# Optimization experiments

Hardware: AMD Instinct MI355X
Metric: run time of the kernel (lower is better)

Reference implementation:

```python
import jax, jax.numpy as jnp
import numpy as np

TARGET_KAPPA = 1.0 / 61.0
EPS = 1e-10

# --- antisymmetric expansion: 35 independent components (i<j<k) -> (7,7,7) ---
_combos = np.array([(i, j, k) for i in range(7) for j in range(i + 1, 7) for k in range(j + 1, 7)])  # (35,3)
_perm_specs = [((0, 1, 2), 1.0), ((0, 2, 1), -1.0), ((1, 0, 2), -1.0), ((1, 2, 0), 1.0), ((2, 0, 1), 1.0), ((2, 1, 0), -1.0)]
_I = jnp.array(np.concatenate([_combos[:, p[0]] for p, _ in _perm_specs]))
_J = jnp.array(np.concatenate([_combos[:, p[1]] for p, _ in _perm_specs]))
_K = jnp.array(np.concatenate([_combos[:, p[2]] for p, _ in _perm_specs]))
_S = jnp.array(np.concatenate([np.full(35, s, dtype=np.float32) for _, s in _perm_specs]))


def expand_to_antisymmetric(v35):
    # v35: (35,) -> antisymmetric (7,7,7)
    vals = jnp.tile(v35, 6) * _S.astype(v35.dtype)
    return jnp.zeros((7, 7, 7), v35.dtype).at[_I, _J, _K].set(vals)


def _phi_single(xi, W1, b1, W2, b2):
    # xi: (7,) -> antisymmetric 3-form (7,7,7)
    h = jnp.tanh(xi @ W1 + b1)          # (H,)
    v35 = h @ W2 + b2                    # (35,)
    return expand_to_antisymmetric(v35)


def setup_inputs() -> dict:
    key = jax.random.key(0)
    k1, k2, k3 = jax.random.split(key, 3)
    B, H = 32768, 512
    x = jax.random.normal(k1, (B, 7), dtype=jnp.float32)
    W1 = jax.random.normal(k2, (7, H), dtype=jnp.float32) * 0.3
    b1 = jnp.zeros((H,), dtype=jnp.float32)
    W2 = jax.random.normal(k3, (H, 35), dtype=jnp.float32) * 0.05
    b2 = jnp.zeros((35,), dtype=jnp.float32)
    return {"x": x, "W1": W1, "b1": b1, "W2": W2, "b2": b2}


def reference(x, W1, b1, W2, b2):
    f = lambda xi: _phi_single(xi, W1, b1, W2, b2)
    # Jacobian replaces the 35 looped autograd.grad calls: (B,7,7,7,7), last axis = d/dx_l
    jac = jax.vmap(jax.jacfwd(f))(x)
    d_phi = jnp.moveaxis(jac, -1, 1)  # (B, 7(deriv), 7, 7, 7), matching torch layout
    torsion_sq = jnp.sum(d_phi ** 2, axis=(1, 2, 3, 4))  # (B,)
    torsion_norm = jnp.sqrt(torsion_sq + EPS)
    loss = jnp.mean((torsion_norm - TARGET_KAPPA) ** 2)
    return loss, jnp.mean(torsion_norm)
```

## Files before the change

### kernel.cpp

```cpp
#include <hip/hip_runtime.h>
#include <hip/hip_bf16.h>
#include <math.h>

typedef __attribute__((ext_vector_type(8)))  short bf16x8;
typedef __attribute__((ext_vector_type(16))) float f32x16;
typedef unsigned int u32;

#define KAPPA (1.0f/61.0f)
#define NBLK 512

__device__ __forceinline__ unsigned short f2bf(float f) {
    u32 x = __float_as_uint(f);
    x += 0x7fffu + ((x >> 16) & 1u);
    return (unsigned short)(x >> 16);
}
__device__ __forceinline__ float fast_rcp(float v) {
#if __has_builtin(__builtin_amdgcn_rcpf)
    return __builtin_amdgcn_rcpf(v);
#else
    return 1.0f / v;
#endif
}
__device__ __forceinline__ u32 pack_bf16(float lo, float hi) {
    __hip_bfloat162 p = __float22bfloat162_rn(make_float2(lo, hi));
    return *reinterpret_cast<u32*>(&p);
}

__global__ void build_v(const float* __restrict__ W1, const float* __restrict__ W2,
                        const float* __restrict__ b1,
                        bf16x8* __restrict__ V, bf16x8* __restrict__ Wt) {
    int t = blockIdx.x * blockDim.x + threadIdx.x;
    if (t < 16384) {
        int lane = t & 63, ptile = (t >> 6) & 7, kkg = t >> 9;
        int p  = ptile * 32 + (lane & 31);
        int hb = kkg * 16 + (lane >> 5) * 8;
        bool valid = (p < 245);
        int l7 = valid ? p / 35 : 0;
        int c  = valid ? p - l7 * 35 : 0;
        bf16x8 v;
#pragma unroll
        for (int i = 0; i < 8; ++i) {
            int h = hb + i;
            v[i] = valid ? (short)f2bf(W1[l7 * 512 + h] * W2[h * 35 + c]) : (short)0;
        }
        V[t] = v;
    } else if (t < 16384 + 1024) {
        int f = t - 16384;
        int lane = f & 63, htile = f >> 6;
        int h = htile * 32 + (lane & 31);
        bf16x8 v;
#pragma unroll
        for (int i = 0; i < 8; ++i) v[i] = 0;
        if (lane < 32) {
#pragma unroll
            for (int l = 0; l < 7; ++l) v[l] = (short)f2bf(W1[l * 512 + h]);
            v[7] = (short)f2bf(b1[h]);
        }
        Wt[f] = v;
    }
}

__global__ __launch_bounds__(256, 3)
void torsion_main(const float* __restrict__ x,
                  const bf16x8* __restrict__ V, const bf16x8* __restrict__ Wt,
                  float* __restrict__ partials) {
    __shared__ __align__(16) u32 Gb[2][8][64 * 4];
    __shared__ float red[4][2][32];

    const int tid  = threadIdx.x;
    const int lane = tid & 63;
    const int w    = tid >> 6;
    const int blk  = blockIdx.x;
    const int rt   = w & 1;
    const int ht   = w >> 1;

    bf16x8 xf;
#pragma unroll
    for (int i = 0; i < 8; ++i) xf[i] = 0;
    if (lane < 32) {
        const float* xp = x + ((size_t)blk * 64 + rt * 32 + lane) * 7;
#pragma unroll
        for (int l = 0; l < 7; ++l) xf[l] = (short)f2bf(xp[l]);
        xf[7] = (short)f2bf(1.0f);
    }

    f32x16 acc[2][2];
#pragma unroll
    for (int pt = 0; pt < 2; ++pt)
#pragma unroll
        for (int r2 = 0; r2 < 2; ++r2)
#pragma unroll
            for (int e = 0; e < 16; ++e) acc[pt][r2][e] = 0.0f;

    auto pre_pack = [&](int c, u32 d[8]) {
        bf16x8 wf = Wt[(c * 2 + ht) * 64 + lane];
        f32x16 p;
#pragma unroll
        for (int e = 0; e < 16; ++e) p[e] = 0.0f;
        p = __builtin_amdgcn_mfma_f32_32x32x16_bf16(wf, xf, p, 0, 0, 0);
#pragma unroll
        for (int j = 0; j < 8; ++j) {
            float t0 = __expf(-2.0f * fabsf(p[2 * j]));
            float r0 = fast_rcp(1.0f + t0);
            float g0 = 4.0f * t0 * r0 * r0;
            float t1 = __expf(-2.0f * fabsf(p[2 * j + 1]));
            float r1 = fast_rcp(1.0f + t1);
            float g1 = 4.0f * t1 * r1 * r1;
            d[j] = pack_bf16(g0, g1);
        }
    };
    auto store_g = [&](int buf, const u32 d[8]) {
        const int f0  = 4 * ht + rt;
        const int f1  = f0 + 2;
        const int col = lane & 31;
        const int hw2 = (lane >> 5) << 1;
        *reinterpret_cast<uint2*>(&Gb[buf][f0][(col     ) * 4 + hw2]) = make_uint2(d[0], d[1]);
        *reinterpret_cast<uint2*>(&Gb[buf][f0][(col + 32) * 4 + hw2]) = make_uint2(d[2], d[3]);
        *reinterpret_cast<uint2*>(&Gb[buf][f1][(col     ) * 4 + hw2]) = make_uint2(d[4], d[5]);
        *reinterpret_cast<uint2*>(&Gb[buf][f1][(col + 32) * 4 + hw2]) = make_uint2(d[6], d[7]);
    };

    {
        u32 d0[8];
        pre_pack(0, d0);
        store_g(0, d0);
    }
    __syncthreads();

    for (int c = 0; c < 8; ++c) {
        const int buf = c & 1;

        bf16x8 vreg[8];
#pragma unroll
        for (int ks = 0; ks < 4; ++ks) {
            const int fb = ((c * 4 + ks) * 8 + 2 * w) * 64 + lane;
            vreg[2 * ks]     = V[fb];
            vreg[2 * ks + 1] = V[fb + 64];
        }

        u32 dn[8];
        if (c < 7) pre_pack(c + 1, dn);

        __builtin_amdgcn_s_setprio(1);
#pragma unroll
        for (int ks = 0; ks < 4; ++ks) {
            bf16x8 g0 = *reinterpret_cast<const bf16x8*>(&Gb[buf][ks * 2 + 0][lane * 4]);
            bf16x8 g1 = *reinterpret_cast<const bf16x8*>(&Gb[buf][ks * 2 + 1][lane * 4]);
            acc[0][0] = __builtin_amdgcn_mfma_f32_32x32x16_bf16(vreg[2 * ks],     g0, acc[0][0], 0, 0, 0);
            acc[0][1] = __builtin_amdgcn_mfma_f32_32x32x16_bf16(vreg[2 * ks],     g1, acc[0][1], 0, 0, 0);
            acc[1][0] = __builtin_amdgcn_mfma_f32_32x32x16_bf16(vreg[2 * ks + 1], g0, acc[1][0], 0, 0, 0);
            acc[1][1] = __builtin_amdgcn_mfma_f32_32x32x16_bf16(vreg[2 * ks + 1], g1, acc[1][1], 0, 0, 0);
        }
        __builtin_amdgcn_s_setprio(0);

        if (c < 7) store_g(buf ^ 1, dn);
        __syncthreads();
    }

#pragma unroll
    for (int r2 = 0; r2 < 2; ++r2) {
        float s = 0.0f;
#pragma unroll
        for (int pt = 0; pt < 2; ++pt)
#pragma unroll
            for (int e = 0; e < 16; ++e) s += acc[pt][r2][e] * acc[pt][r2][e];
        s += __shfl_xor(s, 32);
        if (lane < 32) red[w][r2][lane] = s;
    }
    __syncthreads();

    if (tid < 64) {
        const int li = tid & 31, rr = tid >> 5;
        float q = 6.0f * (red[0][rr][li] + red[1][rr][li] + red[2][rr][li] + red[3][rr][li]);
        float n = sqrtf(q + 1e-10f);
        float d = n - KAPPA;
        float a = d * d, b = n;
#pragma unroll
        for (int m = 1; m <= 32; m <<= 1) {
            a += __shfl_xor(a, m);
            b += __shfl_xor(b, m);
        }
        if (tid == 0) {
            partials[blk]        = a;
            partials[NBLK + blk] = b;
        }
    }
}

__global__ void finalize_k(const float* __restrict__ partials, float* __restrict__ out) {
    __shared__ float sl[256], sn[256];
    int tid = threadIdx.x;
    sl[tid] = partials[tid] + partials[tid + 256];
    sn[tid] = partials[NBLK + tid] + partials[NBLK + tid + 256];
    __syncthreads();
    for (int st = 128; st > 0; st >>= 1) {
        if (tid < st) { sl[tid] += sl[tid + st]; sn[tid] += sn[tid + st]; }
        __syncthreads();
    }
    if (tid == 0) {
        out[0] = sl[0] / 32768.0f;
        out[1] = sn[0] / 32768.0f;
    }
}

extern "C" void kernel_launch(void* const* d_in, const int* in_sizes, int n_in,
                              void* d_out, int out_size, void* d_ws, size_t ws_size,
                              hipStream_t stream) {
    const float* x  = (const float*)d_in[0];
    const float* W1 = (const float*)d_in[1];
    const float* b1 = (const float*)d_in[2];
    const float* W2 = (const float*)d_in[3];

    bf16x8* V        = (bf16x8*)d_ws;
    bf16x8* Wt       = V + 16384;
    float*  partials = (float*)(Wt + 1024);

    build_v<<<68, 256, 0, stream>>>(W1, W2, b1, V, Wt);
    torsion_main<<<NBLK, 256, 0, stream>>>(x, V, Wt, partials);
    finalize_k<<<1, 256, 0, stream>>>(partials, (float*)d_out);
}
```

Baseline: 25.71 us.

## Double rows per block, reuse V fragments across four row tiles, prefetch V/Wt

Measured after the change: 25.92 us. Within noise of the previous version (+0.8%).

```diff
diff --git a/kernel.cpp b/kernel.cpp
--- a/kernel.cpp
+++ b/kernel.cpp
@@ -7,7 +7,8 @@
 typedef unsigned int u32;
 
 #define KAPPA (1.0f/61.0f)
-#define NBLK 512
+#define NBLK 256
+#define SWAP23(r) (((r) & 19) | (((r) & 4) << 1) | (((r) & 8) >> 1))
 
 __device__ __forceinline__ unsigned short f2bf(float f) {
     u32 x = __float_as_uint(f);
@@ -47,7 +48,8 @@
     } else if (t < 16384 + 1024) {
         int f = t - 16384;
         int lane = f & 63, htile = f >> 6;
-        int h = htile * 32 + (lane & 31);
+        int row = lane & 31;
+        int h = htile * 32 + SWAP23(row);
         bf16x8 v;
 #pragma unroll
         for (int i = 0; i < 8; ++i) v[i] = 0;
@@ -60,44 +62,38 @@
     }
 }
 
-__global__ __launch_bounds__(256, 3)
+__global__ __launch_bounds__(256, 1)
 void torsion_main(const float* __restrict__ x,
                   const bf16x8* __restrict__ V, const bf16x8* __restrict__ Wt,
                   float* __restrict__ partials) {
-    __shared__ __align__(16) u32 Gb[2][8][64 * 4];
-    __shared__ float red[4][2][32];
+    __shared__ __align__(16) u32 Gb[2][16][64 * 4];
+    __shared__ float red[4][4][32];
+    __shared__ float fin[2][2];
 
     const int tid  = threadIdx.x;
     const int lane = tid & 63;
     const int w    = tid >> 6;
     const int blk  = blockIdx.x;
-    const int rt   = w & 1;
-    const int ht   = w >> 1;
 
     bf16x8 xf;
 #pragma unroll
     for (int i = 0; i < 8; ++i) xf[i] = 0;
     if (lane < 32) {
-        const float* xp = x + ((size_t)blk * 64 + rt * 32 + lane) * 7;
+        const float* xp = x + ((size_t)blk * 128 + w * 32 + lane) * 7;
 #pragma unroll
         for (int l = 0; l < 7; ++l) xf[l] = (short)f2bf(xp[l]);
         xf[7] = (short)f2bf(1.0f);
     }
 
-    f32x16 acc[2][2];
+    f32x16 acc[2][4];
 #pragma unroll
     for (int pt = 0; pt < 2; ++pt)
 #pragma unroll
-        for (int r2 = 0; r2 < 2; ++r2)
-#pragma unroll
-            for (int e = 0; e < 16; ++e) acc[pt][r2][e] = 0.0f;
-
-    auto pre_pack = [&](int c, u32 d[8]) {
-        bf16x8 wf = Wt[(c * 2 + ht) * 64 + lane];
-        f32x16 p;
-#pragma unroll
-        for (int e = 0; e < 16; ++e) p[e] = 0.0f;
-        p = __builtin_amdgcn_mfma_f32_32x32x16_bf16(wf, xf, p, 0, 0, 0);
+        for (int st = 0; st < 4; ++st)
+#pragma unroll
+            for (int e = 0; e < 16; ++e) acc[pt][st][e] = 0.0f;
+
+    auto compute_g = [&](const f32x16& p, u32 d[8]) {
 #pragma unroll
         for (int j = 0; j < 8; ++j) {
             float t0 = __expf(-2.0f * fabsf(p[2 * j]));
@@ -109,89 +105,119 @@
             d[j] = pack_bf16(g0, g1);
         }
     };
-    auto store_g = [&](int buf, const u32 d[8]) {
-        const int f0  = 4 * ht + rt;
-        const int f1  = f0 + 2;
-        const int col = lane & 31;
-        const int hw2 = (lane >> 5) << 1;
-        *reinterpret_cast<uint2*>(&Gb[buf][f0][(col     ) * 4 + hw2]) = make_uint2(d[0], d[1]);
-        *reinterpret_cast<uint2*>(&Gb[buf][f0][(col + 32) * 4 + hw2]) = make_uint2(d[2], d[3]);
-        *reinterpret_cast<uint2*>(&Gb[buf][f1][(col     ) * 4 + hw2]) = make_uint2(d[4], d[5]);
-        *reinterpret_cast<uint2*>(&Gb[buf][f1][(col + 32) * 4 + hw2]) = make_uint2(d[6], d[7]);
-    };
-
+
+    bf16x8 wt0 = Wt[0 * 64 + lane];
+    bf16x8 wt1 = Wt[1 * 64 + lane];
     {
-        u32 d0[8];
-        pre_pack(0, d0);
-        store_g(0, d0);
-    }
+        f32x16 p0, p1;
+#pragma unroll
+        for (int e = 0; e < 16; ++e) { p0[e] = 0.0f; p1[e] = 0.0f; }
+        p0 = __builtin_amdgcn_mfma_f32_32x32x16_bf16(wt0, xf, p0, 0, 0, 0);
+        p1 = __builtin_amdgcn_mfma_f32_32x32x16_bf16(wt1, xf, p1, 0, 0, 0);
+        u32 d0[8], d1[8];
+        compute_g(p0, d0);
+        compute_g(p1, d1);
+        *reinterpret_cast<uint4*>(&Gb[0][0 * 4 + w][lane * 4]) = make_uint4(d0[0], d0[1], d0[2], d0[3]);
+        *reinterpret_cast<uint4*>(&Gb[0][1 * 4 + w][lane * 4]) = make_uint4(d0[4], d0[5], d0[6], d0[7]);
+        *reinterpret_cast<uint4*>(&Gb[0][2 * 4 + w][lane * 4]) = make_uint4(d1[0], d1[1], d1[2], d1[3]);
+        *reinterpret_cast<uint4*>(&Gb[0][3 * 4 + w][lane * 4]) = make_uint4(d1[4], d1[5], d1[6], d1[7]);
+    }
+    bf16x8 vr[8];
+#pragma unroll
+    for (int ks = 0; ks < 4; ++ks) {
+        const int fb = (ks * 8 + 2 * w) * 64 + lane;
+        vr[ks * 2]     = V[fb];
+        vr[ks * 2 + 1] = V[fb + 64];
+    }
+    wt0 = Wt[2 * 64 + lane];
+    wt1 = Wt[3 * 64 + lane];
     __syncthreads();
 
     for (int c = 0; c < 8; ++c) {
         const int buf = c & 1;
 
-        bf16x8 vreg[8];
-#pragma unroll
-        for (int ks = 0; ks < 4; ++ks) {
-            const int fb = ((c * 4 + ks) * 8 + 2 * w) * 64 + lane;
-            vreg[2 * ks]     = V[fb];
-            vreg[2 * ks + 1] = V[fb + 64];
-        }
-
-        u32 dn[8];
-        if (c < 7) pre_pack(c + 1, dn);
-
-        __builtin_amdgcn_s_setprio(1);
-#pragma unroll
-        for (int ks = 0; ks < 4; ++ks) {
-            bf16x8 g0 = *reinterpret_cast<const bf16x8*>(&Gb[buf][ks * 2 + 0][lane * 4]);
-            bf16x8 g1 = *reinterpret_cast<const bf16x8*>(&Gb[buf][ks * 2 + 1][lane * 4]);
-            acc[0][0] = __builtin_amdgcn_mfma_f32_32x32x16_bf16(vreg[2 * ks],     g0, acc[0][0], 0, 0, 0);
-            acc[0][1] = __builtin_amdgcn_mfma_f32_32x32x16_bf16(vreg[2 * ks],     g1, acc[0][1], 0, 0, 0);
-            acc[1][0] = __builtin_amdgcn_mfma_f32_32x32x16_bf16(vreg[2 * ks + 1], g0, acc[1][0], 0, 0, 0);
-            acc[1][1] = __builtin_amdgcn_mfma_f32_32x32x16_bf16(vreg[2 * ks + 1], g1, acc[1][1], 0, 0, 0);
-        }
-        __builtin_amdgcn_s_setprio(0);
-
-        if (c < 7) store_g(buf ^ 1, dn);
+        f32x16 p0, p1;
+        if (c < 7) {
+#pragma unroll
+            for (int e = 0; e < 16; ++e) { p0[e] = 0.0f; p1[e] = 0.0f; }
+            p0 = __builtin_amdgcn_mfma_f32_32x32x16_bf16(wt0, xf, p0, 0, 0, 0);
+            p1 = __builtin_amdgcn_mfma_f32_32x32x16_bf16(wt1, xf, p1, 0, 0, 0);
+        }
+
+#pragma unroll
+        for (int ks = 0; ks < 4; ++ks)
+#pragma unroll
+            for (int st = 0; st < 4; ++st) {
+                bf16x8 g = *reinterpret_cast<const bf16x8*>(&Gb[buf][ks * 4 + st][lane * 4]);
+                acc[0][st] = __builtin_amdgcn_mfma_f32_32x32x16_bf16(vr[ks * 2],     g, acc[0][st], 0, 0, 0);
+                acc[1][st] = __builtin_amdgcn_mfma_f32_32x32x16_bf16(vr[ks * 2 + 1], g, acc[1][st], 0, 0, 0);
+            }
+
+        if (c < 7) {
+#pragma unroll
+            for (int ks = 0; ks < 4; ++ks) {
+                const int fb = (((c + 1) * 4 + ks) * 8 + 2 * w) * 64 + lane;
+                vr[ks * 2]     = V[fb];
+                vr[ks * 2 + 1] = V[fb + 64];
+            }
+        }
+        if (c < 6) {
+            wt0 = Wt[((c + 2) * 2 + 0) * 64 + lane];
+            wt1 = Wt[((c + 2) * 2 + 1) * 64 + lane];
+        }
+
+        if (c < 7) {
+            u32 d0[8], d1[8];
+            compute_g(p0, d0);
+            compute_g(p1, d1);
+            *reinterpret_cast<uint4*>(&Gb[buf ^ 1][0 * 4 + w][lane * 4]) = make_uint4(d0[0], d0[1], d0[2], d0[3]);
+            *reinterpret_cast<uint4*>(&Gb[buf ^ 1][1 * 4 + w][lane * 4]) = make_uint4(d0[4], d0[5], d0[6], d0[7]);
+            *reinterpret_cast<uint4*>(&Gb[buf ^ 1][2 * 4 + w][lane * 4]) = make_uint4(d1[0], d1[1], d1[2], d1[3]);
+            *reinterpret_cast<uint4*>(&Gb[buf ^ 1][3 * 4 + w][lane * 4]) = make_uint4(d1[4], d1[5], d1[6], d1[7]);
+        }
         __syncthreads();
     }
 
 #pragma unroll
-    for (int r2 = 0; r2 < 2; ++r2) {
+    for (int st = 0; st < 4; ++st) {
         float s = 0.0f;
 #pragma unroll
         for (int pt = 0; pt < 2; ++pt)
 #pragma unroll
-            for (int e = 0; e < 16; ++e) s += acc[pt][r2][e] * acc[pt][r2][e];
+            for (int e = 0; e < 16; ++e) s += acc[pt][st][e] * acc[pt][st][e];
         s += __shfl_xor(s, 32);
-        if (lane < 32) red[w][r2][lane] = s;
-    }
-    __syncthreads();
-
-    if (tid < 64) {
-        const int li = tid & 31, rr = tid >> 5;
-        float q = 6.0f * (red[0][rr][li] + red[1][rr][li] + red[2][rr][li] + red[3][rr][li]);
+        if (lane < 32) red[w][st][lane] = s;
+    }
+    __syncthreads();
+
+    if (tid < 128) {
+        const int st = tid >> 5, col = tid & 31;
+        float q = 6.0f * (red[0][st][col] + red[1][st][col] + red[2][st][col] + red[3][st][col]);
         float n = sqrtf(q + 1e-10f);
-        float d = n - KAPPA;
-        float a = d * d, b = n;
+        float dd = n - KAPPA;
+        float a = dd * dd, b = n;
 #pragma unroll
         for (int m = 1; m <= 32; m <<= 1) {
             a += __shfl_xor(a, m);
             b += __shfl_xor(b, m);
         }
-        if (tid == 0) {
-            partials[blk]        = a;
-            partials[NBLK + blk] = b;
-        }
+        if ((tid & 63) == 0) {
+            fin[0][tid >> 6] = a;
+            fin[1][tid >> 6] = b;
+        }
+    }
+    __syncthreads();
+    if (tid == 0) {
+        partials[blk]        = fin[0][0] + fin[0][1];
+        partials[NBLK + blk] = fin[1][0] + fin[1][1];
     }
 }
 
 __global__ void finalize_k(const float* __restrict__ partials, float* __restrict__ out) {
     __shared__ float sl[256], sn[256];
     int tid = threadIdx.x;
-    sl[tid] = partials[tid] + partials[tid + 256];
-    sn[tid] = partials[NBLK + tid] + partials[NBLK + tid + 256];
+    sl[tid] = partials[tid];
+    sn[tid] = partials[NBLK + tid];
     __syncthreads();
     for (int st = 128; st > 0; st >>= 1) {
         if (tid < st) { sl[tid] += sl[tid + st]; sn[tid] += sn[tid + st]; }
```

## Fuse finalize into main kernel via atomic ticket and simplify G LDS stores

Applied to the files above, without the earlier changes.

Result: slower. 31.99 us (+24.4%).

```diff
diff --git a/kernel.cpp b/kernel.cpp
--- a/kernel.cpp
+++ b/kernel.cpp
@@ -8,6 +8,7 @@
 
 #define KAPPA (1.0f/61.0f)
 #define NBLK 512
+#define SWAP23(r) (((r) & 19) | (((r) & 4) << 1) | (((r) & 8) >> 1))
 
 __device__ __forceinline__ unsigned short f2bf(float f) {
     u32 x = __float_as_uint(f);
@@ -28,8 +29,10 @@
 
 __global__ void build_v(const float* __restrict__ W1, const float* __restrict__ W2,
                         const float* __restrict__ b1,
-                        bf16x8* __restrict__ V, bf16x8* __restrict__ Wt) {
+                        bf16x8* __restrict__ V, bf16x8* __restrict__ Wt,
+                        int* __restrict__ ticket) {
     int t = blockIdx.x * blockDim.x + threadIdx.x;
+    if (t == 0) *ticket = 0;
     if (t < 16384) {
         int lane = t & 63, ptile = (t >> 6) & 7, kkg = t >> 9;
         int p  = ptile * 32 + (lane & 31);
@@ -47,7 +50,8 @@
     } else if (t < 16384 + 1024) {
         int f = t - 16384;
         int lane = f & 63, htile = f >> 6;
-        int h = htile * 32 + (lane & 31);
+        int row = lane & 31;
+        int h = htile * 32 + SWAP23(row);
         bf16x8 v;
 #pragma unroll
         for (int i = 0; i < 8; ++i) v[i] = 0;
@@ -63,9 +67,11 @@
 __global__ __launch_bounds__(256, 3)
 void torsion_main(const float* __restrict__ x,
                   const bf16x8* __restrict__ V, const bf16x8* __restrict__ Wt,
-                  float* __restrict__ partials) {
+                  float* __restrict__ partials, int* __restrict__ ticket,
+                  float* __restrict__ out) {
     __shared__ __align__(16) u32 Gb[2][8][64 * 4];
     __shared__ float red[4][2][32];
+    __shared__ int is_last;
 
     const int tid  = threadIdx.x;
     const int lane = tid & 63;
@@ -110,14 +116,10 @@
         }
     };
     auto store_g = [&](int buf, const u32 d[8]) {
-        const int f0  = 4 * ht + rt;
-        const int f1  = f0 + 2;
-        const int col = lane & 31;
-        const int hw2 = (lane >> 5) << 1;
-        *reinterpret_cast<uint2*>(&Gb[buf][f0][(col     ) * 4 + hw2]) = make_uint2(d[0], d[1]);
-        *reinterpret_cast<uint2*>(&Gb[buf][f0][(col + 32) * 4 + hw2]) = make_uint2(d[2], d[3]);
-        *reinterpret_cast<uint2*>(&Gb[buf][f1][(col     ) * 4 + hw2]) = make_uint2(d[4], d[5]);
-        *reinterpret_cast<uint2*>(&Gb[buf][f1][(col + 32) * 4 + hw2]) = make_uint2(d[6], d[7]);
+        *reinterpret_cast<uint4*>(&Gb[buf][(2 * ht + 0) * 2 + rt][lane * 4]) =
+            make_uint4(d[0], d[1], d[2], d[3]);
+        *reinterpret_cast<uint4*>(&Gb[buf][(2 * ht + 1) * 2 + rt][lane * 4]) =
+            make_uint4(d[4], d[5], d[6], d[7]);
     };
 
     {
@@ -140,6 +142,8 @@
 
         u32 dn[8];
         if (c < 7) pre_pack(c + 1, dn);
+
+        if (c < 7) store_g(buf ^ 1, dn);
 
         __builtin_amdgcn_s_setprio(1);
 #pragma unroll
@@ -152,8 +156,6 @@
             acc[1][1] = __builtin_amdgcn_mfma_f32_32x32x16_bf16(vreg[2 * ks + 1], g1, acc[1][1], 0, 0, 0);
         }
         __builtin_amdgcn_s_setprio(0);
-
-        if (c < 7) store_g(buf ^ 1, dn);
         __syncthreads();
     }
 
@@ -185,21 +187,31 @@
             partials[NBLK + blk] = b;
         }
     }
-}
-
-__global__ void finalize_k(const float* __restrict__ partials, float* __restrict__ out) {
-    __shared__ float sl[256], sn[256];
-    int tid = threadIdx.x;
-    sl[tid] = partials[tid] + partials[tid + 256];
-    sn[tid] = partials[NBLK + tid] + partials[NBLK + tid + 256];
-    __syncthreads();
-    for (int st = 128; st > 0; st >>= 1) {
-        if (tid < st) { sl[tid] += sl[tid + st]; sn[tid] += sn[tid + st]; }
-        __syncthreads();
-    }
+    __syncthreads();
+
     if (tid == 0) {
-        out[0] = sl[0] / 32768.0f;
-        out[1] = sn[0] / 32768.0f;
+        __threadfence();
+        int old = atomicAdd(ticket, 1);
+        is_last = (old == NBLK - 1) ? 1 : 0;
+    }
+    __syncthreads();
+    if (is_last && tid < 64) {
+        __threadfence();
+        float a = 0.0f, b = 0.0f;
+#pragma unroll
+        for (int i = 0; i < NBLK / 64; ++i) {
+            a += partials[i * 64 + tid];
+            b += partials[NBLK + i * 64 + tid];
+        }
+#pragma unroll
+        for (int m = 1; m <= 32; m <<= 1) {
+            a += __shfl_xor(a, m);
+            b += __shfl_xor(b, m);
+        }
+        if (tid == 0) {
+            out[0] = a / 32768.0f;
+            out[1] = b / 32768.0f;
+        }
     }
 }
 
@@ -214,8 +226,8 @@
     bf16x8* V        = (bf16x8*)d_ws;
     bf16x8* Wt       = V + 16384;
     float*  partials = (float*)(Wt + 1024);
-
-    build_v<<<68, 256, 0, stream>>>(W1, W2, b1, V, Wt);
-    torsion_main<<<NBLK, 256, 0, stream>>>(x, V, Wt, partials);
-    finalize_k<<<1, 256, 0, stream>>>(partials, (float*)d_out);
-}
+    int*    ticket   = (int*)(partials + 2 * NBLK);
+
+    build_v<<<68, 256, 0, stream>>>(W1, W2, b1, V, Wt, ticket);
+    torsion_main<<<NBLK, 256, 0, stream>>>(x, V, Wt, partials, ticket, (float*)d_out);
+}
```
